# Kernel tuning notes

Hardware: AMD Instinct MI355X
Metric: run time of the kernel (lower is better)

Reference implementation:

```python
import jax, jax.numpy as jnp
import numpy as np

B, N, L, D, V = 32, 2048, 128, 1024, 32000

def setup_inputs() -> dict:
    key = jax.random.key(0)
    k1, k2, k3 = jax.random.split(key, 3)
    image_features = jax.random.normal(k1, (B, N, D), dtype=jnp.float32)
    token_ids = jax.random.randint(k2, (B, L), 0, V, dtype=jnp.int64)
    emb_table = jax.random.normal(k3, (V, D), dtype=jnp.float32)
    return {"image_features": image_features, "token_ids": token_ids, "emb_table": emb_table}

def reference(image_features, token_ids, emb_table):
    # targets = embeddings(input_ids): [B, L, D]
    targets = emb_table[token_ids]
    # batched pairwise L2 distance (torch.cdist p=2): ||x-y|| via the
    # expanded form ||x||^2 + ||y||^2 - 2<x,y>, clamped for numerical safety.
    x2 = jnp.sum(image_features * image_features, axis=-1)        # [B, N]
    y2 = jnp.sum(targets * targets, axis=-1)                      # [B, L]
    xy = jnp.einsum('bnd,bld->bnl', image_features, targets)      # [B, N, L]
    d2 = x2[:, :, None] + y2[:, None, :] - 2.0 * xy
    costs = jnp.sqrt(jnp.maximum(d2, 0.0))                        # [B, N, L]
    smallest = jnp.min(costs, axis=-1)                            # [B, N]
    return smallest.mean()
```

## Files before the change

### kernel.cpp

```cpp
#include <hip/hip_runtime.h>
#include <cstdint>
#include <cstddef>

#define BATCH 32
#define NROW  2048
#define LTOK  128
#define DDIM  1024

typedef short s8v  __attribute__((ext_vector_type(8)));
typedef float f4v  __attribute__((ext_vector_type(4)));

__device__ __forceinline__ uint32_t pk2(float lo, float hi) {
    return __builtin_amdgcn_perm(__float_as_uint(hi), __float_as_uint(lo), 0x07060302u);
}

__global__ __launch_bounds__(256)
void prep_y(const int*   __restrict__ tok,
            const float* __restrict__ E,
            uint32_t*    __restrict__ Ybf,
            float*       __restrict__ y2)
{
    const int l = blockIdx.x, b = blockIdx.y;
    const int tid = threadIdx.x;
    const int t = tok[b * LTOK + l];
    const float4 v = ((const float4*)(E + (size_t)t * DDIM))[tid];
    float s = v.x*v.x + v.y*v.y + v.z*v.z + v.w*v.w;
    uint2 p; p.x = pk2(v.x, v.y); p.y = pk2(v.z, v.w);
    ((uint2*)(Ybf + ((size_t)(b * LTOK + l) * DDIM) / 2))[tid] = p;
#pragma unroll
    for (int o = 1; o < 64; o <<= 1) s += __shfl_xor(s, o);
    __shared__ float ws4[4];
    if ((tid & 63) == 0) ws4[tid >> 6] = s;
    __syncthreads();
    if (tid == 0) y2[b * LTOK + l] = ws4[0] + ws4[1] + ws4[2] + ws4[3];
}

__global__ __launch_bounds__(256, 4)
void cdist_min_mean_kernel(const float* __restrict__ X,
                           const short* __restrict__ Ybf,
                           const float* __restrict__ y2g,
                           float* __restrict__ out)
{
    __shared__ __align__(16) short Ys[LTOK * 128];
    __shared__ float x2s[64];
    __shared__ float rowmin[64];

    const int tid  = threadIdx.x;
    const int lane = tid & 63;
    const int wid  = tid >> 6;
    const int quad = lane >> 4;
    const int l15  = lane & 15;
    const int rxor = l15 & 7;

    const int b       = blockIdx.y;
    const int rowBase = blockIdx.x * 64;

    const float* xptr = X + ((size_t)b * NROW + rowBase + wid * 16 + l15) * DDIM + quad * 8;

    const short* ysrc = Ybf + ((size_t)b * LTOK + (tid >> 4)) * DDIM
                      + (((tid & 15) ^ ((tid >> 4) & 7)) * 8);

    f4v acc[8];
#pragma unroll
    for (int ni = 0; ni < 8; ++ni) acc[ni] = (f4v){0.f, 0.f, 0.f, 0.f};
    float xacc = 0.f;

    float4 pa[4], pb[4];
#pragma unroll
    for (int t = 0; t < 3; ++t) {
        pa[t] = *(const float4*)(xptr + t * 32);
        pb[t] = *(const float4*)(xptr + t * 32 + 4);
    }

#pragma unroll
    for (int t = 0; t < 32; ++t) {
        if ((t & 3) == 0) {
            const int e = t >> 2;
            if (t) __syncthreads();
#pragma unroll
            for (int i = 0; i < 8; ++i)
                __builtin_amdgcn_global_load_lds(
                    (const __attribute__((address_space(1))) void*)
                        (ysrc + (size_t)i * 16 * DDIM + e * 128),
                    (__attribute__((address_space(3))) void*)
                        &Ys[(i * 256 + (wid << 6)) * 8],
                    16, 0, 0);
            __syncthreads();
        }

        const float4 a = pa[t & 3], c = pb[t & 3];
        xacc += a.x*a.x + a.y*a.y + a.z*a.z + a.w*a.w
              + c.x*c.x + c.y*c.y + c.z*c.z + c.w*c.w;
        uint4 p;
        p.x = pk2(a.x, a.y); p.y = pk2(a.z, a.w);
        p.z = pk2(c.x, c.y); p.w = pk2(c.z, c.w);
        s8v af;
        __builtin_memcpy(&af, &p, 16);

        if (t + 3 < 32) {
            pa[(t + 3) & 3] = *(const float4*)(xptr + (t + 3) * 32);
            pb[(t + 3) & 3] = *(const float4*)(xptr + (t + 3) * 32 + 4);
        }

        const int ksl = t & 3;
#pragma unroll
        for (int ni = 0; ni < 8; ++ni) {
            const s8v bf = *(const s8v*)&Ys[(ni * 16 + l15) * 128
                                            + (((ksl * 4 + quad) ^ rxor) * 8)];
            acc[ni] = __builtin_amdgcn_mfma_f32_16x16x32_bf16(af, bf, acc[ni], 0, 0, 0);
        }
    }

    {
        float s = xacc;
        s += __shfl_xor(s, 16);
        s += __shfl_xor(s, 32);
        if (lane < 16) x2s[wid * 16 + lane] = s;
    }

    float y2r[8];
#pragma unroll
    for (int ni = 0; ni < 8; ++ni)
        y2r[ni] = y2g[b * LTOK + ni * 16 + l15];

#pragma unroll
    for (int j = 0; j < 4; ++j) {
        float m = y2r[0] - 2.f * acc[0][j];
#pragma unroll
        for (int ni = 1; ni < 8; ++ni)
            m = fminf(m, y2r[ni] - 2.f * acc[ni][j]);
        m = fminf(m, __shfl_xor(m, 1));
        m = fminf(m, __shfl_xor(m, 2));
        m = fminf(m, __shfl_xor(m, 4));
        m = fminf(m, __shfl_xor(m, 8));
        if (l15 == 0) rowmin[wid * 16 + quad * 4 + j] = m;
    }
    __syncthreads();

    if (tid < 64) {
        float part = sqrtf(fmaxf(x2s[tid] + rowmin[tid], 0.f));
#pragma unroll
        for (int s = 1; s < 64; s <<= 1) part += __shfl_xor(part, s);
        if (tid == 0)
            atomicAdd(out, part * (1.0f / (float)(BATCH * NROW)));
    }
}

extern "C" void kernel_launch(void* const* d_in, const int* in_sizes, int n_in,
                              void* d_out, int out_size, void* d_ws, size_t ws_size,
                              hipStream_t stream) {
    const float* X   = (const float*)d_in[0];
    const int*   tok = (const int*)d_in[1];
    const float* E   = (const float*)d_in[2];
    float* out = (float*)d_out;

    uint32_t* Ybf = (uint32_t*)d_ws;
    float*    y2  = (float*)((char*)d_ws + (size_t)BATCH * LTOK * DDIM * 2);

    hipMemsetAsync(out, 0, sizeof(float), stream);

    dim3 pgrid(LTOK, BATCH, 1);
    prep_y<<<pgrid, 256, 0, stream>>>(tok, E, Ybf, y2);

    dim3 grid(NROW / 64, BATCH, 1);
    cdist_min_mean_kernel<<<grid, 256, 0, stream>>>(X, (const short*)Ybf, y2, out);
}
```

Before: 427.6 us.

## Double-buffer Y tiles in LDS and remap blocks for L2 locality

Replaces the single 128-column Y staging buffer, which needed a full sync before and after each load, with two 64-column LDS buffers. The next stage's global-to-LDS load is issued before computing the current one, using explicit vmcnt waits and s_barrier instead of __syncthreads. Also remaps the block index so consecutive workgroups spread across batches, presumably for L2 or XCD locality. The hand-counted vmcnt values depend on the exact load ordering the compiler emits and are fragile if it changes.

Result: no change. 433.9 us (+1.5%).

```diff
diff --git a/kernel.cpp b/kernel.cpp
--- a/kernel.cpp
+++ b/kernel.cpp
@@ -6,6 +6,9 @@
 #define NROW  2048
 #define LTOK  128
 #define DDIM  1024
+
+#define NSTG  16
+#define SCOL  64
 
 typedef short s8v  __attribute__((ext_vector_type(8)));
 typedef float f4v  __attribute__((ext_vector_type(4)));
@@ -41,7 +44,7 @@
                            const float* __restrict__ y2g,
                            float* __restrict__ out)
 {
-    __shared__ __align__(16) short Ys[LTOK * 128];
+    __shared__ __align__(16) short Ys[2][LTOK * SCOL];
     __shared__ float x2s[64];
     __shared__ float rowmin[64];
 
@@ -52,13 +55,18 @@
     const int l15  = lane & 15;
     const int rxor = l15 & 7;
 
-    const int b       = blockIdx.y;
-    const int rowBase = blockIdx.x * 64;
+    const int linear  = blockIdx.y * gridDim.x + blockIdx.x;
+    const int newlin  = (linear & 7) * 128 + (linear >> 3);
+    const int b       = newlin >> 5;
+    const int rowBase = (newlin & 31) * 64;
 
     const float* xptr = X + ((size_t)b * NROW + rowBase + wid * 16 + l15) * DDIM + quad * 8;
 
-    const short* ysrc = Ybf + ((size_t)b * LTOK + (tid >> 4)) * DDIM
-                      + (((tid & 15) ^ ((tid >> 4) & 7)) * 8);
+    const short* ysrc[4];
+#pragma unroll
+    for (int i = 0; i < 4; ++i)
+        ysrc[i] = Ybf + ((size_t)b * LTOK + i * 32 + wid * 8 + (lane >> 3)) * DDIM
+                + (((lane & 7) ^ (lane >> 3)) << 3);
 
     f4v acc[8];
 #pragma unroll
@@ -66,28 +74,17 @@
     float xacc = 0.f;
 
     float4 pa[4], pb[4];
+
+    auto stage = [&](int st, int buf) {
 #pragma unroll
-    for (int t = 0; t < 3; ++t) {
-        pa[t] = *(const float4*)(xptr + t * 32);
-        pb[t] = *(const float4*)(xptr + t * 32 + 4);
-    }
+        for (int i = 0; i < 4; ++i)
+            __builtin_amdgcn_global_load_lds(
+                (const __attribute__((address_space(1))) void*)(ysrc[i] + st * SCOL),
+                (__attribute__((address_space(3))) void*)&Ys[buf][(i * 256 + (wid << 6)) * 8],
+                16, 0, 0);
+    };
 
-#pragma unroll
-    for (int t = 0; t < 32; ++t) {
-        if ((t & 3) == 0) {
-            const int e = t >> 2;
-            if (t) __syncthreads();
-#pragma unroll
-            for (int i = 0; i < 8; ++i)
-                __builtin_amdgcn_global_load_lds(
-                    (const __attribute__((address_space(1))) void*)
-                        (ysrc + (size_t)i * 16 * DDIM + e * 128),
-                    (__attribute__((address_space(3))) void*)
-                        &Ys[(i * 256 + (wid << 6)) * 8],
-                    16, 0, 0);
-            __syncthreads();
-        }
-
+    auto chunk = [&](int t, int buf) {
         const float4 a = pa[t & 3], c = pb[t & 3];
         xacc += a.x*a.x + a.y*a.y + a.z*a.z + a.w*a.w
               + c.x*c.x + c.y*c.y + c.z*c.z + c.w*c.w;
@@ -102,12 +99,36 @@
             pb[(t + 3) & 3] = *(const float4*)(xptr + (t + 3) * 32 + 4);
         }
 
-        const int ksl = t & 3;
+        const int t2 = t & 1;
 #pragma unroll
         for (int ni = 0; ni < 8; ++ni) {
-            const s8v bf = *(const s8v*)&Ys[(ni * 16 + l15) * 128
-                                            + (((ksl * 4 + quad) ^ rxor) * 8)];
+            const s8v bf = *(const s8v*)&Ys[buf][(ni * 16 + l15) * SCOL
+                                                + (((t2 * 4 + quad) ^ rxor) << 3)];
             acc[ni] = __builtin_amdgcn_mfma_f32_16x16x32_bf16(af, bf, acc[ni], 0, 0, 0);
+        }
+    };
+
+    stage(0, 0);
+#pragma unroll
+    for (int t = 0; t < 3; ++t) {
+        pa[t] = *(const float4*)(xptr + t * 32);
+        pb[t] = *(const float4*)(xptr + t * 32 + 4);
+    }
+    __builtin_amdgcn_sched_barrier(0);
+    asm volatile("s_waitcnt vmcnt(6)" ::: "memory");
+    __builtin_amdgcn_s_barrier();
+
+#pragma unroll
+    for (int st = 0; st < NSTG; ++st) {
+        const int buf = st & 1;
+        if (st < NSTG - 1) stage(st + 1, buf ^ 1);
+        chunk(2 * st,     buf);
+        chunk(2 * st + 1, buf);
+        if (st < NSTG - 1) {
+            __builtin_amdgcn_sched_barrier(0);
+            if (st == NSTG - 2) asm volatile("s_waitcnt vmcnt(2)" ::: "memory");
+            else                asm volatile("s_waitcnt vmcnt(4)" ::: "memory");
+            __builtin_amdgcn_s_barrier();
         }
     }
 
```
